# Kernel tuning notes

Measured on AMD Instinct MI355X. Metric: run time of the kernel, lower is better.

Reference implementation:

```python
import jax, jax.numpy as jnp
import numpy as np

N, K = 10000, 16
EDGE_DIM, HID = 32, 64
MULT = 8            # rep1.mult == rep2.mult (out_mult)
NL = 2              # lvals [0,1] -> 2 irreps per rep
DIM = 4             # (2*0+1) + (2*1+1)
NHEADS = 4
OUT3 = 3 * MULT     # qkv multiplicity
RW_FLAT = NL * NL * MULT * OUT3   # 768 radial-weight outputs per edge
HEAD_DIM = (MULT * DIM) // NHEADS # 8
INDICES = jnp.array([0, 1, 1, 1]) # irrep index for each of the DIM slots (l=0 then l=1 x3)


def setup_inputs() -> dict:
    key = jax.random.key(0)
    ks = jax.random.split(key, 10)
    rn = lambda i, shape, sc=1.0: (jax.random.normal(ks[i], shape, jnp.float32) * sc)
    return {
        "b1": rn(0, (N, K, DIM, NL)),
        "b2": rn(1, (N, K, NL, DIM)),
        "edge_feats": rn(2, (N, K, EDGE_DIM)),
        "f": rn(3, (N, MULT, DIM)),
        "neighbor_idx": jax.random.randint(ks[4], (N, K), 0, N),
        # RadialWeight MLP params (xavier-ish scales, zero biases as in _init_weights)
        "W1": rn(5, (HID, EDGE_DIM), (2.0 / (HID + EDGE_DIM)) ** 0.5),
        "b1_lin": jnp.zeros((HID,), jnp.float32),
        "W2": rn(6, (RW_FLAT, HID), (2.0 / (RW_FLAT + HID)) ** 0.5),
        "b2_lin": jnp.zeros((RW_FLAT,), jnp.float32),
        # EquivariantLinear out_proj params
        "W_out": rn(7, (NL * MULT, MULT), (2.0 / (NL * MULT + MULT)) ** 0.5),
        "bias_out": jnp.zeros((MULT, 1), jnp.float32),
    }


def reference(b1, b2, edge_feats, f, neighbor_idx, W1, b1_lin, W2, b2_lin, W_out, bias_out):
    E = N * K
    b1f = b1.reshape(E, DIM, NL)
    b2f = b2.reshape(E, NL, DIM)
    ef = edge_feats.reshape(E, EDGE_DIM)

    # RadialWeight: 2-layer MLP with exact GELU -> per-edge tensor-product weights
    h = jax.nn.gelu(ef @ W1.T + b1_lin, approximate=False)          # (E, HID)
    rw = (h @ W2.T + b2_lin).reshape(E, NL * OUT3, NL * MULT)        # (E, 48, 16)

    # EquivariantConvolution: gather src node features, chained small matmuls
    f_src = f[neighbor_idx.reshape(-1)]                              # (E, MULT, DIM)
    tmp = jnp.einsum('emd,edl->eml', f_src, b1f)                     # (E, MULT, NL)
    tmp = jnp.matmul(rw, tmp.reshape(E, NL * MULT, 1))               # (E, NL*OUT3, 1)
    qkv = jnp.matmul(tmp.reshape(E, OUT3, NL), b2f)                  # (E, OUT3, DIM)

    # split into q,k,v heads
    qkv = qkv.reshape(N, K, 3 * MULT, DIM)
    q, k_, v = jnp.split(qkv, 3, axis=2)                             # each (N, K, MULT, DIM)
    qh = q.reshape(N, K, NHEADS, HEAD_DIM)
    kh = k_.reshape(N, K, NHEADS, HEAD_DIM)
    vh = v.reshape(N, K, NHEADS, HEAD_DIM)

    # per-edge attention, softmax over the k neighbors
    scale = HEAD_DIM ** -0.5
    scores = jnp.einsum('nkhd,nkhd->nkh', qh, kh) * scale            # (N, K, NHEADS)
    attn = jax.nn.softmax(scores, axis=1)
    out = jnp.einsum('nkh,nkhd->nhd', attn, vh).reshape(N, MULT, DIM)

    # EquivariantLinear out_proj: per-irrep mixing over multiplicity channels
    o = jnp.einsum('om,nmd->nod', W_out, out).reshape(N, NL, MULT, DIM)
    idx = jnp.broadcast_to(INDICES[None, None, None, :], (N, 1, MULT, DIM))
    o = jnp.take_along_axis(o, idx, axis=1)[:, 0]                    # (N, MULT, DIM)
    # bias only on the scalar (l=0) slot; activation is Identity in out_proj
    o = o.at[:, :, 0].add(bias_out[:, 0])
    return o
```

## Files before the change

### kernel.cpp

```cpp
#include <hip/hip_runtime.h>
#include <math.h>

#define E_TOT   160000
#define TPB     64
#define NBLK    (E_TOT / TPB)
#define TV_OFF  8192
#define T2S     52
#define SMEM_SZ 13312

typedef __attribute__((ext_vector_type(8))) __bf16 bf16x8;
typedef __attribute__((ext_vector_type(4))) float f32x4;

static __device__ __forceinline__ unsigned short f2bf(float v) {
    unsigned int u = __float_as_uint(v);
    u += 0x7FFFu + ((u >> 16) & 1u);
    return (unsigned short)(u >> 16);
}
static __device__ __forceinline__ float bf2f(unsigned int s) {
    return __uint_as_float(s << 16);
}

static __device__ __forceinline__ float gelu_exact(float a) {
    float x = a * 0.70710678118654752f;
    float s = fabsf(x);
    float t = __builtin_amdgcn_rcpf(fmaf(0.3275911f, s, 1.0f));
    float p = fmaf(1.061405429f, t, -1.453152027f);
    p = fmaf(p, t, 1.421413741f);
    p = fmaf(p, t, -0.284496736f);
    p = fmaf(p, t, 0.254829592f);
    p = p * t;
    float er = fmaf(-p, __expf(-s * s), 1.0f);
    er = copysignf(er, x);
    return 0.5f * a * (1.0f + er);
}

__global__ __launch_bounds__(256) void w_split(
    const float* __restrict__ W2, const float* __restrict__ b2l,
    uint4* __restrict__ hi4, uint4* __restrict__ lo4, uint4* __restrict__ bb4)
{
    const int c = blockIdx.x * 256 + threadIdx.x;
    if (c < 6144) {
        const int lane = c & 63, rest = c >> 6;
        const int kk   = rest & 1, tj = rest >> 1;
        const int j    = tj & 15,  t  = tj >> 4;
        const int grp  = lane >> 4, r16 = lane & 15;
        const float* src = W2 + (size_t)((t * 16 + r16) * 16 + j) * 64 + kk * 32 + grp * 8;
        union { uint4 u; unsigned short s[8]; } H, L;
        #pragma unroll
        for (int i = 0; i < 8; ++i) {
            float w = src[i];
            unsigned short h = f2bf(w);
            H.s[i] = h;
            L.s[i] = f2bf(w - bf2f(h));
        }
        hi4[c] = H.u;
        lo4[c] = L.u;
    } else if (c < 6144 + 192) {
        const int cc   = c - 6144;
        const int lane = cc & 63, t = cc >> 6;
        const int grp  = lane >> 4, r16 = lane & 15;
        union { uint4 u; unsigned short s[8]; } B;
        #pragma unroll
        for (int i = 0; i < 8; ++i)
            B.s[i] = (grp < 2) ? f2bf(b2l[(t * 16 + r16) * 16 + grp * 8 + i])
                               : (unsigned short)0;
        bb4[cc] = B.u;
    }
}

__global__ __launch_bounds__(TPB) void eq_attn_kernel(
    const float* __restrict__ b1,
    const float* __restrict__ b2,
    const float* __restrict__ ef,
    const float* __restrict__ f,
    const int*   __restrict__ nidx,
    const float* __restrict__ W1,
    const float* __restrict__ b1l,
    const float* __restrict__ Wout,
    const float* __restrict__ bias,
    const uint4* __restrict__ wsh,
    const uint4* __restrict__ wsl,
    const uint4* __restrict__ bb,
    float* __restrict__ out)
{
    __shared__ unsigned char smem[SMEM_SZ];
    const int tid = threadIdx.x;
    const int e   = blockIdx.x * TPB + tid;
    const int r16 = tid & 15;
    const int grp = tid >> 4;

    float efr[32];
    {
        const float4* ef4 = reinterpret_cast<const float4*>(ef + (size_t)e * 32);
        #pragma unroll
        for (int i = 0; i < 8; ++i) {
            float4 v = ef4[i];
            efr[i*4+0] = v.x; efr[i*4+1] = v.y; efr[i*4+2] = v.z; efr[i*4+3] = v.w;
        }
    }
    uint4 Hc[8], Lc[8];
    {
        #pragma unroll
        for (int c8 = 0; c8 < 8; ++c8) {
            union { uint4 u; unsigned short s[8]; } H, L;
            #pragma unroll
            for (int i = 0; i < 8; ++i) {
                const int hid = c8 * 8 + i;
                float acc = b1l[hid];
                #pragma unroll
                for (int c = 0; c < 32; ++c)
                    acc = fmaf(efr[c], W1[hid * 32 + c], acc);
                float v = gelu_exact(acc);
                unsigned short hs = f2bf(v);
                H.s[i] = hs;
                L.s[i] = f2bf(v - bf2f(hs));
            }
            Hc[c8] = H.u;
            Lc[c8] = L.u;
        }
        #pragma unroll
        for (int c8 = 0; c8 < 8; ++c8)
            *(uint4*)(smem + tid * 128 + ((c8 ^ (tid & 7)) * 16)) = Hc[c8];
    }
    float tmpv[16];
    {
        const int src = nidx[e];
        float fs[32];
        const float4* f4 = reinterpret_cast<const float4*>(f + (size_t)src * 32);
        #pragma unroll
        for (int i = 0; i < 8; ++i) {
            float4 v = f4[i];
            fs[i*4+0] = v.x; fs[i*4+1] = v.y; fs[i*4+2] = v.z; fs[i*4+3] = v.w;
        }
        float b1r[8];
        const float4* b14 = reinterpret_cast<const float4*>(b1 + (size_t)e * 8);
        float4 u0 = b14[0], u1 = b14[1];
        b1r[0]=u0.x; b1r[1]=u0.y; b1r[2]=u0.z; b1r[3]=u0.w;
        b1r[4]=u1.x; b1r[5]=u1.y; b1r[6]=u1.z; b1r[7]=u1.w;
        float* tvp = (float*)(smem + TV_OFF);
        #pragma unroll
        for (int m = 0; m < 8; ++m) {
            float a0 = 0.f, a1 = 0.f;
            #pragma unroll
            for (int d = 0; d < 4; ++d) {
                a0 = fmaf(fs[m*4+d], b1r[d*2+0], a0);
                a1 = fmaf(fs[m*4+d], b1r[d*2+1], a1);
            }
            tmpv[m*2+0] = a0; tmpv[m*2+1] = a1;
            tvp[(m*2+0) * 64 + tid] = a0;
            tvp[(m*2+1) * 64 + tid] = a1;
        }
    }

    __syncthreads();
    bf16x8 Ahi[4][2], Alo[4][2];
    #pragma unroll
    for (int mt = 0; mt < 4; ++mt)
        #pragma unroll
        for (int kk = 0; kk < 2; ++kk) {
            const int row = mt * 16 + r16;
            const int ch  = (kk * 4 + grp) ^ (r16 & 7);
            Ahi[mt][kk] = *(const bf16x8*)(smem + row * 128 + ch * 16);
        }
    __syncthreads();
    #pragma unroll
    for (int c8 = 0; c8 < 8; ++c8)
        *(uint4*)(smem + tid * 128 + ((c8 ^ (tid & 7)) * 16)) = Lc[c8];
    __syncthreads();
    #pragma unroll
    for (int mt = 0; mt < 4; ++mt)
        #pragma unroll
        for (int kk = 0; kk < 2; ++kk) {
            const int row = mt * 16 + r16;
            const int ch  = (kk * 4 + grp) ^ (r16 & 7);
            Alo[mt][kk] = *(const bf16x8*)(smem + row * 128 + ch * 16);
        }
    __syncthreads();

    f32x4 acc[4][3];
    {
        const float* tvp = (const float*)(smem + TV_OFF);
        bf16x8 tvb[4];
        #pragma unroll
        for (int mt = 0; mt < 4; ++mt) {
            union { uint4 u; unsigned short s[8]; } P;
            #pragma unroll
            for (int i = 0; i < 8; ++i) {
                float v = (grp < 2) ? tvp[(grp * 8 + i) * 64 + mt * 16 + r16] : 0.0f;
                P.s[i] = f2bf(v);
            }
            tvb[mt] = *(bf16x8*)&P.u;
        }
        bf16x8 blb[3];
        #pragma unroll
        for (int t = 0; t < 3; ++t) {
            uint4 u = bb[t * 64 + tid];
            blb[t] = *(bf16x8*)&u;
        }
        #pragma unroll
        for (int mt = 0; mt < 4; ++mt)
            #pragma unroll
            for (int t = 0; t < 3; ++t)
                acc[mt][t] = __builtin_amdgcn_mfma_f32_16x16x32_bf16(
                    tvb[mt], blb[t], (f32x4){0.f, 0.f, 0.f, 0.f}, 0, 0, 0);
    }

    const float4* tv4 = (const float4*)(smem + TV_OFF);
    #pragma unroll 4
    for (int j = 0; j < 16; ++j) {
        bf16x8 Bhi[3][2], Blo[3][2];
        #pragma unroll
        for (int t = 0; t < 3; ++t)
            #pragma unroll
            for (int kk = 0; kk < 2; ++kk) {
                const int chunk = ((t * 16 + j) * 2 + kk) * 64 + tid;
                Bhi[t][kk] = ((const bf16x8*)wsh)[chunk];
                Blo[t][kk] = ((const bf16x8*)wsl)[chunk];
            }
        #pragma unroll
        for (int mt = 0; mt < 4; ++mt) {
            float4 tv = tv4[j * 16 + mt * 4 + grp];
            #pragma unroll
            for (int t = 0; t < 3; ++t) {
                f32x4 rw = (f32x4){0.f, 0.f, 0.f, 0.f};
                rw = __builtin_amdgcn_mfma_f32_16x16x32_bf16(Ahi[mt][0], Bhi[t][0], rw, 0, 0, 0);
                rw = __builtin_amdgcn_mfma_f32_16x16x32_bf16(Ahi[mt][1], Bhi[t][1], rw, 0, 0, 0);
                rw = __builtin_amdgcn_mfma_f32_16x16x32_bf16(Alo[mt][0], Bhi[t][0], rw, 0, 0, 0);
                rw = __builtin_amdgcn_mfma_f32_16x16x32_bf16(Alo[mt][1], Bhi[t][1], rw, 0, 0, 0);
                rw = __builtin_amdgcn_mfma_f32_16x16x32_bf16(Ahi[mt][0], Blo[t][0], rw, 0, 0, 0);
                rw = __builtin_amdgcn_mfma_f32_16x16x32_bf16(Ahi[mt][1], Blo[t][1], rw, 0, 0, 0);
                acc[mt][t].x = fmaf(tv.x, rw.x, acc[mt][t].x);
                acc[mt][t].y = fmaf(tv.y, rw.y, acc[mt][t].y);
                acc[mt][t].z = fmaf(tv.z, rw.z, acc[mt][t].z);
                acc[mt][t].w = fmaf(tv.w, rw.w, acc[mt][t].w);
            }
        }
    }

    __syncthreads();
    {
        float* t2p = (float*)smem;
        #pragma unroll
        for (int mt = 0; mt < 4; ++mt) {
            const int eb = mt * 16 + grp * 4;
            #pragma unroll
            for (int t = 0; t < 3; ++t) {
                t2p[(eb + 0) * T2S + t * 16 + r16] = acc[mt][t].x;
                t2p[(eb + 1) * T2S + t * 16 + r16] = acc[mt][t].y;
                t2p[(eb + 2) * T2S + t * 16 + r16] = acc[mt][t].z;
                t2p[(eb + 3) * T2S + t * 16 + r16] = acc[mt][t].w;
            }
        }
    }
    __syncthreads();

    float t2[48];
    {
        const float* t2r = (const float*)smem + (size_t)tid * T2S;
        #pragma unroll
        for (int o2 = 0; o2 < 48; ++o2) t2[o2] = t2r[o2];
    }

    float b2r[8];
    {
        const float4* b24 = reinterpret_cast<const float4*>(b2 + (size_t)e * 8);
        float4 u0 = b24[0], u1 = b24[1];
        b2r[0]=u0.x; b2r[1]=u0.y; b2r[2]=u0.z; b2r[3]=u0.w;
        b2r[4]=u1.x; b2r[5]=u1.y; b2r[6]=u1.z; b2r[7]=u1.w;
    }
    float q[8][4];
    #pragma unroll
    for (int o = 0; o < 8; ++o) {
        float t0 = t2[2*o+0], t1 = t2[2*o+1];
        #pragma unroll
        for (int d = 0; d < 4; ++d)
            q[o][d] = fmaf(t0, b2r[d], t1 * b2r[4+d]);
    }
    float scores[4] = {0.f, 0.f, 0.f, 0.f};
    #pragma unroll
    for (int o = 0; o < 8; ++o) {
        float t0 = t2[16+2*o+0], t1 = t2[16+2*o+1];
        float sacc = 0.f;
        #pragma unroll
        for (int d = 0; d < 4; ++d) {
            float kr = fmaf(t0, b2r[d], t1 * b2r[4+d]);
            sacc = fmaf(q[o][d], kr, sacc);
        }
        scores[o >> 1] += sacc;
    }
    float vv[8][4];
    #pragma unroll
    for (int o = 0; o < 8; ++o) {
        float t0 = t2[32+2*o+0], t1 = t2[32+2*o+1];
        #pragma unroll
        for (int d = 0; d < 4; ++d)
            vv[o][d] = fmaf(t0, b2r[d], t1 * b2r[4+d]);
    }

    float attn[4];
    #pragma unroll
    for (int hh = 0; hh < 4; ++hh) {
        float s = scores[hh] * 0.35355339059327373f;
        float mx = s;
        #pragma unroll
        for (int msk = 8; msk; msk >>= 1)
            mx = fmaxf(mx, __shfl_xor(mx, msk, 16));
        float p = __expf(s - mx);
        float ps = p;
        #pragma unroll
        for (int msk = 8; msk; msk >>= 1)
            ps += __shfl_xor(ps, msk, 16);
        attn[hh] = p / ps;
    }

    float osum[8][4];
    #pragma unroll
    for (int m = 0; m < 8; ++m) {
        float w = attn[m >> 1];
        #pragma unroll
        for (int d = 0; d < 4; ++d) {
            float val = w * vv[m][d];
            #pragma unroll
            for (int msk = 8; msk; msk >>= 1)
                val += __shfl_xor(val, msk, 16);
            osum[m][d] = val;
        }
    }

    if ((tid & 15) == 0) {
        const int n = e >> 4;
        #pragma unroll
        for (int od = 0; od < 8; ++od) {
            #pragma unroll
            for (int d = 0; d < 4; ++d) {
                const int row = (d == 0) ? od : (8 + od);
                float a = (d == 0) ? bias[od] : 0.f;
                #pragma unroll
                for (int m = 0; m < 8; ++m)
                    a = fmaf(Wout[row * 8 + m], osum[m][d], a);
                out[(size_t)n * 32 + od * 4 + d] = a;
            }
        }
    }
}

extern "C" void kernel_launch(void* const* d_in, const int* in_sizes, int n_in,
                              void* d_out, int out_size, void* d_ws, size_t ws_size,
                              hipStream_t stream) {
    const float* b1   = (const float*)d_in[0];
    const float* b2   = (const float*)d_in[1];
    const float* ef   = (const float*)d_in[2];
    const float* f    = (const float*)d_in[3];
    const int*   nidx = (const int*)d_in[4];
    const float* W1   = (const float*)d_in[5];
    const float* b1l  = (const float*)d_in[6];
    const float* W2   = (const float*)d_in[7];
    const float* b2l  = (const float*)d_in[8];
    const float* Wout = (const float*)d_in[9];
    const float* bias = (const float*)d_in[10];
    float* out = (float*)d_out;

    uint4* wsh = (uint4*)d_ws;
    uint4* wsl = wsh + 6144;
    uint4* bb  = wsh + 12288;

    hipLaunchKernelGGL(w_split, dim3(25), dim3(256), 0, stream, W2, b2l, wsh, wsl, bb);
    hipLaunchKernelGGL(eq_attn_kernel, dim3(NBLK), dim3(TPB), 0, stream,
                       b1, b2, ef, f, nidx, W1, b1l, Wout, bias,
                       (const uint4*)wsh, (const uint4*)wsl, (const uint4*)bb, out);
}
```

Baseline: 193.4 us.

## Split each 64-edge tile across four waves with K-split MFMA and LDS reduction

Each block now has 256 threads (four waves) working on the same 64 edges. The hidden-layer computation is divided by hidden chunk, and the W2 MFMA loop is split over j, so each wave handles a quarter of the K dimension. Partial accumulators are summed in LDS across waves in a rotated order with barriers, and each wave then runs the attention epilogue for 16 edges. The goal is more parallelism and latency hiding per edge tile, and hi/lo LDS staging now avoids the extra sync round. The costs are extra barriers, LDS read-modify-write reductions, and an epilogue that uses only a quarter of the lanes.

```diff
diff --git a/kernel.cpp b/kernel.cpp
--- a/kernel.cpp
+++ b/kernel.cpp
@@ -2,11 +2,12 @@
 #include <math.h>
 
 #define E_TOT   160000
-#define TPB     64
-#define NBLK    (E_TOT / TPB)
-#define TV_OFF  8192
+#define BE      64
+#define TPB     256
+#define NBLK    (E_TOT / BE)
+#define TV_OFF  16384
 #define T2S     52
-#define SMEM_SZ 13312
+#define SMEM_SZ 20480
 
 typedef __attribute__((ext_vector_type(8))) __bf16 bf16x8;
 typedef __attribute__((ext_vector_type(4))) float f32x4;
@@ -68,7 +69,7 @@
     }
 }
 
-__global__ __launch_bounds__(TPB) void eq_attn_kernel(
+__global__ __launch_bounds__(TPB, 2) void eq_attn_kernel(
     const float* __restrict__ b1,
     const float* __restrict__ b2,
     const float* __restrict__ ef,
@@ -85,23 +86,24 @@
 {
     __shared__ unsigned char smem[SMEM_SZ];
     const int tid = threadIdx.x;
-    const int e   = blockIdx.x * TPB + tid;
-    const int r16 = tid & 15;
-    const int grp = tid >> 4;
-
-    float efr[32];
+    const int p   = tid >> 6;
+    const int el  = tid & 63;
+    const int r16 = el & 15;
+    const int grp = el >> 4;
+    const int e0  = blockIdx.x * BE;
+    const int e   = e0 + el;
+
     {
+        float efr[32];
         const float4* ef4 = reinterpret_cast<const float4*>(ef + (size_t)e * 32);
         #pragma unroll
         for (int i = 0; i < 8; ++i) {
             float4 v = ef4[i];
             efr[i*4+0] = v.x; efr[i*4+1] = v.y; efr[i*4+2] = v.z; efr[i*4+3] = v.w;
         }
-    }
-    uint4 Hc[8], Lc[8];
-    {
-        #pragma unroll
-        for (int c8 = 0; c8 < 8; ++c8) {
+        #pragma unroll
+        for (int cc = 0; cc < 2; ++cc) {
+            const int c8 = 2 * p + cc;
             union { uint4 u; unsigned short s[8]; } H, L;
             #pragma unroll
             for (int i = 0; i < 8; ++i) {
@@ -115,15 +117,12 @@
                 H.s[i] = hs;
                 L.s[i] = f2bf(v - bf2f(hs));
             }
-            Hc[c8] = H.u;
-            Lc[c8] = L.u;
-        }
-        #pragma unroll
-        for (int c8 = 0; c8 < 8; ++c8)
-            *(uint4*)(smem + tid * 128 + ((c8 ^ (tid & 7)) * 16)) = Hc[c8];
-    }
-    float tmpv[16];
-    {
+            const int ch = c8 ^ (el & 7);
+            *(uint4*)(smem +        el * 128 + ch * 16) = H.u;
+            *(uint4*)(smem + 8192 + el * 128 + ch * 16) = L.u;
+        }
+    }
+    if (p == 0) {
         const int src = nidx[e];
         float fs[32];
         const float4* f4 = reinterpret_cast<const float4*>(f + (size_t)src * 32);
@@ -146,13 +145,13 @@
                 a0 = fmaf(fs[m*4+d], b1r[d*2+0], a0);
                 a1 = fmaf(fs[m*4+d], b1r[d*2+1], a1);
             }
-            tmpv[m*2+0] = a0; tmpv[m*2+1] = a1;
-            tvp[(m*2+0) * 64 + tid] = a0;
-            tvp[(m*2+1) * 64 + tid] = a1;
+            tvp[(m*2+0) * 64 + el] = a0;
+            tvp[(m*2+1) * 64 + el] = a1;
         }
     }
 
     __syncthreads();
+
     bf16x8 Ahi[4][2], Alo[4][2];
     #pragma unroll
     for (int mt = 0; mt < 4; ++mt)
@@ -160,25 +159,12 @@
         for (int kk = 0; kk < 2; ++kk) {
             const int row = mt * 16 + r16;
             const int ch  = (kk * 4 + grp) ^ (r16 & 7);
-            Ahi[mt][kk] = *(const bf16x8*)(smem + row * 128 + ch * 16);
-        }
-    __syncthreads();
-    #pragma unroll
-    for (int c8 = 0; c8 < 8; ++c8)
-        *(uint4*)(smem + tid * 128 + ((c8 ^ (tid & 7)) * 16)) = Lc[c8];
-    __syncthreads();
-    #pragma unroll
-    for (int mt = 0; mt < 4; ++mt)
-        #pragma unroll
-        for (int kk = 0; kk < 2; ++kk) {
-            const int row = mt * 16 + r16;
-            const int ch  = (kk * 4 + grp) ^ (r16 & 7);
-            Alo[mt][kk] = *(const bf16x8*)(smem + row * 128 + ch * 16);
-        }
-    __syncthreads();
+            Ahi[mt][kk] = *(const bf16x8*)(smem +        row * 128 + ch * 16);
+            Alo[mt][kk] = *(const bf16x8*)(smem + 8192 + row * 128 + ch * 16);
+        }
 
     f32x4 acc[4][3];
-    {
+    if (p == 0) {
         const float* tvp = (const float*)(smem + TV_OFF);
         bf16x8 tvb[4];
         #pragma unroll
@@ -194,7 +180,7 @@
         bf16x8 blb[3];
         #pragma unroll
         for (int t = 0; t < 3; ++t) {
-            uint4 u = bb[t * 64 + tid];
+            uint4 u = bb[t * 64 + el];
             blb[t] = *(bf16x8*)&u;
         }
         #pragma unroll
@@ -203,17 +189,24 @@
             for (int t = 0; t < 3; ++t)
                 acc[mt][t] = __builtin_amdgcn_mfma_f32_16x16x32_bf16(
                     tvb[mt], blb[t], (f32x4){0.f, 0.f, 0.f, 0.f}, 0, 0, 0);
+    } else {
+        #pragma unroll
+        for (int mt = 0; mt < 4; ++mt)
+            #pragma unroll
+            for (int t = 0; t < 3; ++t)
+                acc[mt][t] = (f32x4){0.f, 0.f, 0.f, 0.f};
     }
 
     const float4* tv4 = (const float4*)(smem + TV_OFF);
-    #pragma unroll 4
-    for (int j = 0; j < 16; ++j) {
+    #pragma unroll
+    for (int jj = 0; jj < 4; ++jj) {
+        const int j = p * 4 + jj;
         bf16x8 Bhi[3][2], Blo[3][2];
         #pragma unroll
         for (int t = 0; t < 3; ++t)
             #pragma unroll
             for (int kk = 0; kk < 2; ++kk) {
-                const int chunk = ((t * 16 + j) * 2 + kk) * 64 + tid;
+                const int chunk = ((t * 16 + j) * 2 + kk) * 64 + el;
                 Bhi[t][kk] = ((const bf16x8*)wsh)[chunk];
                 Blo[t][kk] = ((const bf16x8*)wsl)[chunk];
             }
@@ -238,107 +231,119 @@
     }
 
     __syncthreads();
+
     {
         float* t2p = (float*)smem;
         #pragma unroll
-        for (int mt = 0; mt < 4; ++mt) {
+        for (int r = 0; r < 4; ++r) {
+            const int mt = (p + r) & 3;
             const int eb = mt * 16 + grp * 4;
-            #pragma unroll
-            for (int t = 0; t < 3; ++t) {
-                t2p[(eb + 0) * T2S + t * 16 + r16] = acc[mt][t].x;
-                t2p[(eb + 1) * T2S + t * 16 + r16] = acc[mt][t].y;
-                t2p[(eb + 2) * T2S + t * 16 + r16] = acc[mt][t].z;
-                t2p[(eb + 3) * T2S + t * 16 + r16] = acc[mt][t].w;
-            }
-        }
-    }
-    __syncthreads();
-
-    float t2[48];
-    {
-        const float* t2r = (const float*)smem + (size_t)tid * T2S;
-        #pragma unroll
-        for (int o2 = 0; o2 < 48; ++o2) t2[o2] = t2r[o2];
-    }
-
-    float b2r[8];
-    {
-        const float4* b24 = reinterpret_cast<const float4*>(b2 + (size_t)e * 8);
-        float4 u0 = b24[0], u1 = b24[1];
-        b2r[0]=u0.x; b2r[1]=u0.y; b2r[2]=u0.z; b2r[3]=u0.w;
-        b2r[4]=u1.x; b2r[5]=u1.y; b2r[6]=u1.z; b2r[7]=u1.w;
-    }
-    float q[8][4];
-    #pragma unroll
-    for (int o = 0; o < 8; ++o) {
-        float t0 = t2[2*o+0], t1 = t2[2*o+1];
-        #pragma unroll
-        for (int d = 0; d < 4; ++d)
-            q[o][d] = fmaf(t0, b2r[d], t1 * b2r[4+d]);
-    }
-    float scores[4] = {0.f, 0.f, 0.f, 0.f};
-    #pragma unroll
-    for (int o = 0; o < 8; ++o) {
-        float t0 = t2[16+2*o+0], t1 = t2[16+2*o+1];
-        float sacc = 0.f;
-        #pragma unroll
-        for (int d = 0; d < 4; ++d) {
-            float kr = fmaf(t0, b2r[d], t1 * b2r[4+d]);
-            sacc = fmaf(q[o][d], kr, sacc);
-        }
-        scores[o >> 1] += sacc;
-    }
-    float vv[8][4];
-    #pragma unroll
-    for (int o = 0; o < 8; ++o) {
-        float t0 = t2[32+2*o+0], t1 = t2[32+2*o+1];
-        #pragma unroll
-        for (int d = 0; d < 4; ++d)
-            vv[o][d] = fmaf(t0, b2r[d], t1 * b2r[4+d]);
-    }
-
-    float attn[4];
-    #pragma unroll
-    for (int hh = 0; hh < 4; ++hh) {
-        float s = scores[hh] * 0.35355339059327373f;
-        float mx = s;
-        #pragma unroll
-        for (int msk = 8; msk; msk >>= 1)
-            mx = fmaxf(mx, __shfl_xor(mx, msk, 16));
-        float p = __expf(s - mx);
-        float ps = p;
-        #pragma unroll
-        for (int msk = 8; msk; msk >>= 1)
-            ps += __shfl_xor(ps, msk, 16);
-        attn[hh] = p / ps;
-    }
-
-    float osum[8][4];
-    #pragma unroll
-    for (int m = 0; m < 8; ++m) {
-        float w = attn[m >> 1];
-        #pragma unroll
-        for (int d = 0; d < 4; ++d) {
-            float val = w * vv[m][d];
+            if (r == 0) {
+                #pragma unroll
+                for (int t = 0; t < 3; ++t) {
+                    t2p[(eb + 0) * T2S + t * 16 + r16] = acc[mt][t].x;
+                    t2p[(eb + 1) * T2S + t * 16 + r16] = acc[mt][t].y;
+                    t2p[(eb + 2) * T2S + t * 16 + r16] = acc[mt][t].z;
+                    t2p[(eb + 3) * T2S + t * 16 + r16] = acc[mt][t].w;
+                }
+            } else {
+                #pragma unroll
+                for (int t = 0; t < 3; ++t) {
+                    t2p[(eb + 0) * T2S + t * 16 + r16] += acc[mt][t].x;
+                    t2p[(eb + 1) * T2S + t * 16 + r16] += acc[mt][t].y;
+                    t2p[(eb + 2) * T2S + t * 16 + r16] += acc[mt][t].z;
+                    t2p[(eb + 3) * T2S + t * 16 + r16] += acc[mt][t].w;
+                }
+            }
+            __syncthreads();
+        }
+    }
+
+    if (el < 16) {
+        const int erow = p * 16 + el;
+        const int ec   = e0 + erow;
+        float t2[48];
+        {
+            const float* t2r = (const float*)smem + (size_t)erow * T2S;
+            #pragma unroll
+            for (int o2 = 0; o2 < 48; ++o2) t2[o2] = t2r[o2];
+        }
+        float b2r[8];
+        {
+            const float4* b24 = reinterpret_cast<const float4*>(b2 + (size_t)ec * 8);
+            float4 u0 = b24[0], u1 = b24[1];
+            b2r[0]=u0.x; b2r[1]=u0.y; b2r[2]=u0.z; b2r[3]=u0.w;
+            b2r[4]=u1.x; b2r[5]=u1.y; b2r[6]=u1.z; b2r[7]=u1.w;
+        }
+        float q[8][4];
+        #pragma unroll
+        for (int o = 0; o < 8; ++o) {
+            float t0 = t2[2*o+0], t1 = t2[2*o+1];
+            #pragma unroll
+            for (int d = 0; d < 4; ++d)
+                q[o][d] = fmaf(t0, b2r[d], t1 * b2r[4+d]);
+        }
+        float scores[4] = {0.f, 0.f, 0.f, 0.f};
+        #pragma unroll
+        for (int o = 0; o < 8; ++o) {
+            float t0 = t2[16+2*o+0], t1 = t2[16+2*o+1];
+            float sacc = 0.f;
+            #pragma unroll
+            for (int d = 0; d < 4; ++d) {
+                float kr = fmaf(t0, b2r[d], t1 * b2r[4+d]);
+                sacc = fmaf(q[o][d], kr, sacc);
+            }
+            scores[o >> 1] += sacc;
+        }
+        float vv[8][4];
+        #pragma unroll
+        for (int o = 0; o < 8; ++o) {
+            float t0 = t2[32+2*o+0], t1 = t2[32+2*o+1];
+            #pragma unroll
+            for (int d = 0; d < 4; ++d)
+                vv[o][d] = fmaf(t0, b2r[d], t1 * b2r[4+d]);
+        }
+        float attn[4];
+        #pragma unroll
+        for (int hh = 0; hh < 4; ++hh) {
+            float s = scores[hh] * 0.35355339059327373f;
+            float mx = s;
             #pragma unroll
             for (int msk = 8; msk; msk >>= 1)
-                val += __shfl_xor(val, msk, 16);
-            osum[m][d] = val;
-        }
-    }
-
-    if ((tid & 15) == 0) {
-        const int n = e >> 4;
-        #pragma unroll
-        for (int od = 0; od < 8; ++od) {
+                mx = fmaxf(mx, __shfl_xor(mx, msk, 16));
+            float pr = __expf(s - mx);
+            float ps = pr;
+            #pragma unroll
+            for (int msk = 8; msk; msk >>= 1)
+                ps += __shfl_xor(ps, msk, 16);
+            attn[hh] = pr / ps;
+        }
+        float osum[8][4];
+        #pragma unroll
+        for (int m = 0; m < 8; ++m) {
+            float w = attn[m >> 1];
             #pragma unroll
             for (int d = 0; d < 4; ++d) {
-                const int row = (d == 0) ? od : (8 + od);
-                float a = (d == 0) ? bias[od] : 0.f;
-                #pragma unroll
-                for (int m = 0; m < 8; ++m)
-                    a = fmaf(Wout[row * 8 + m], osum[m][d], a);
-                out[(size_t)n * 32 + od * 4 + d] = a;
+                float val = w * vv[m][d];
+                #pragma unroll
+                for (int msk = 8; msk; msk >>= 1)
+                    val += __shfl_xor(val, msk, 16);
+                osum[m][d] = val;
+            }
+        }
+        if (el == 0) {
+            const int n = ec >> 4;
+            #pragma unroll
+            for (int od = 0; od < 8; ++od) {
+                #pragma unroll
+                for (int d = 0; d < 4; ++d) {
+                    const int row = (d == 0) ? od : (8 + od);
+                    float a = (d == 0) ? bias[od] : 0.f;
+                    #pragma unroll
+                    for (int m = 0; m < 8; ++m)
+                        a = fmaf(Wout[row * 8 + m], osum[m][d], a);
+                    out[(size_t)n * 32 + od * 4 + d] = a;
+                }
             }
         }
     }
```

Measured after the change: 275.9 us. 42.7% more time.
